# Performance work log

Hardware: AMD Instinct MI355X
Metric: run time of the kernel (lower is better)

Reference implementation:

```python
import jax, jax.numpy as jnp
import numpy as np

E, B, D, T = 8, 4096, 2048, 2048
H = D // 2 + T // 2  # expert hidden dim = 2048
TOP_K = 2


def setup_inputs() -> dict:
    key = jax.random.key(0)
    ks = jax.random.split(key, 5)
    s_in = 1.0 / np.sqrt(D)
    s_h = 1.0 / np.sqrt(H)
    return {
        "xs": jax.random.normal(ks[0], (E, B, D), dtype=jnp.float32),
        "Wg": jax.random.normal(ks[1], (D,), dtype=jnp.float32) * s_in,
        "bg": jnp.zeros((1,), dtype=jnp.float32),
        "W1": jax.random.normal(ks[2], (E, D, H), dtype=jnp.float32) * s_in,
        "b1": jnp.zeros((E, H), dtype=jnp.float32),
        "W2": jax.random.normal(ks[3], (E, H, T), dtype=jnp.float32) * s_h,
        "b2": jnp.zeros((E, T), dtype=jnp.float32),
    }


def reference(xs, Wg, bg, W1, b1, W2, b2):
    # Gating: logits[b, e] = x[e][b] @ Wg + bg  -> [B, E]
    logits = jnp.einsum("ebd,d->be", xs, Wg) + bg
    probs = jax.nn.softmax(logits, axis=1)
    top_k_values, top_k_indices = jax.lax.top_k(probs, TOP_K)  # [B, K]

    # Dense expert compute over each expert's own input stream.
    # hidden[e, b, h] = relu(x[e] @ W1[e] + b1[e]); out[e, b, t] = hidden @ W2[e] + b2[e]
    hidden = jax.nn.relu(jnp.einsum("ebd,edh->ebh", xs, W1) + b1[:, None, :])
    expert_out = jnp.einsum("ebh,eht->ebt", hidden, W2) + b2[:, None, :]  # [E, B, T]

    # Gather the top-k experts per token. In the original, masked-dense compute
    # + output mask is mathematically identical to this gather.
    per_token = jnp.transpose(expert_out, (1, 0, 2))  # [B, E, T]
    selected = jnp.take_along_axis(per_token, top_k_indices[:, :, None], axis=1)  # [B, K, T]

    out = jnp.sum(top_k_values[:, :, None] * selected, axis=1)  # [B, T]
    return out, top_k_values
```

## Files before the change

kernel.cpp:

```cpp
#include <hip/hip_runtime.h>
#include <hip/hip_bf16.h>
#include <stdint.h>

#define E_ 8
#define B_ 4096
#define D_ 2048
#define T_ 2048
#define H_ 2048
#define KDIM 2048
#define NDIM 2048

typedef __attribute__((ext_vector_type(4))) float f32x4;
typedef __attribute__((ext_vector_type(4))) unsigned short u16x4;
typedef __attribute__((ext_vector_type(8))) unsigned short u16x8;
typedef __attribute__((ext_vector_type(8))) __bf16 bf16x8;

__device__ __forceinline__ unsigned short f2bf(float f) {
    __hip_bfloat16 h = __float2bfloat16(f);
    return __builtin_bit_cast(unsigned short, h);
}

__device__ __forceinline__ void gload_lds16(const void* g, void* lds) {
    __builtin_amdgcn_global_load_lds(
        (const __attribute__((address_space(1))) void*)g,
        (__attribute__((address_space(3))) void*)lds, 16, 0, 0);
}

__global__ __launch_bounds__(256) void moe_gating(
    const float* __restrict__ xs, const float* __restrict__ Wg,
    const float* __restrict__ bg, float* __restrict__ out_topk,
    float* __restrict__ prob_slot, int* __restrict__ counts,
    int* __restrict__ slot_of, unsigned short* __restrict__ A1)
{
    const int b = blockIdx.x;
    const int t = threadIdx.x;
    const int wave = t >> 6, lane = t & 63;
    __shared__ float red[E_][4];
    __shared__ int sh_i0, sh_i1;

    const f32x4 wg0 = ((const f32x4*)Wg)[t];
    const f32x4 wg1 = ((const f32x4*)Wg)[t + 256];

    f32x4 xa[E_], xb[E_];
    #pragma unroll
    for (int e = 0; e < E_; ++e) {
        const f32x4* xr = (const f32x4*)(xs + ((size_t)e * B_ + b) * D_);
        xa[e] = __builtin_nontemporal_load(&xr[t]);
        xb[e] = __builtin_nontemporal_load(&xr[t + 256]);
        float p = xa[e].x*wg0.x + xa[e].y*wg0.y + xa[e].z*wg0.z + xa[e].w*wg0.w
                + xb[e].x*wg1.x + xb[e].y*wg1.y + xb[e].z*wg1.z + xb[e].w*wg1.w;
        #pragma unroll
        for (int off = 32; off >= 1; off >>= 1) p += __shfl_xor(p, off);
        if (lane == 0) red[e][wave] = p;
    }
    __syncthreads();
    if (t == 0) {
        float pr[E_];
        float mx = -3.0e38f;
        #pragma unroll
        for (int e = 0; e < E_; ++e) {
            pr[e] = red[e][0] + red[e][1] + red[e][2] + red[e][3] + bg[0];
            mx = fmaxf(mx, pr[e]);
        }
        float s = 0.f;
        #pragma unroll
        for (int e = 0; e < E_; ++e) { pr[e] = expf(pr[e] - mx); s += pr[e]; }
        float inv = 1.0f / s;
        #pragma unroll
        for (int e = 0; e < E_; ++e) pr[e] *= inv;
        int i0 = 0;
        #pragma unroll
        for (int e = 1; e < E_; ++e) if (pr[e] > pr[i0]) i0 = e;
        int i1 = (i0 == 0) ? 1 : 0;
        #pragma unroll
        for (int e = 0; e < E_; ++e) { if (e != i0 && pr[e] > pr[i1]) i1 = e; }
        float p0 = pr[i0], p1 = pr[i1];
        out_topk[2*b]    = p0;
        out_topk[2*b+1]  = p1;
        prob_slot[2*b]   = p0;
        prob_slot[2*b+1] = p1;
        int pos0 = atomicAdd(&counts[i0], 1);
        slot_of[i0 * B_ + pos0] = 2*b;
        int pos1 = atomicAdd(&counts[i1], 1);
        slot_of[i1 * B_ + pos1] = 2*b + 1;
        sh_i0 = i0; sh_i1 = i1;
    }
    __syncthreads();
    const int i0 = sh_i0, i1 = sh_i1;
    f32x4 s0a = xa[0], s0b = xb[0], s1a = xa[0], s1b = xb[0];
    #pragma unroll
    for (int e = 0; e < E_; ++e) {
        if (i0 == e) { s0a = xa[e]; s0b = xb[e]; }
        if (i1 == e) { s1a = xa[e]; s1b = xb[e]; }
    }
    u16x4 w;
    w[0]=f2bf(s0a.x); w[1]=f2bf(s0a.y); w[2]=f2bf(s0a.z); w[3]=f2bf(s0a.w);
    ((u16x4*)(A1 + (size_t)(2*b) * D_))[t] = w;
    w[0]=f2bf(s0b.x); w[1]=f2bf(s0b.y); w[2]=f2bf(s0b.z); w[3]=f2bf(s0b.w);
    ((u16x4*)(A1 + (size_t)(2*b) * D_ + 1024))[t] = w;
    w[0]=f2bf(s1a.x); w[1]=f2bf(s1a.y); w[2]=f2bf(s1a.z); w[3]=f2bf(s1a.w);
    ((u16x4*)(A1 + (size_t)(2*b+1) * D_))[t] = w;
    w[0]=f2bf(s1b.x); w[1]=f2bf(s1b.y); w[2]=f2bf(s1b.z); w[3]=f2bf(s1b.w);
    ((u16x4*)(A1 + (size_t)(2*b+1) * D_ + 1024))[t] = w;
}

__global__ void build_tiles(const int* __restrict__ counts, int* __restrict__ tiles)
{
    if (threadIdx.x == 0 && blockIdx.x == 0) {
        int n = 0;
        for (int e = 0; e < E_; ++e) {
            int te = (counts[e] + 127) >> 7;
            for (int m = 0; m < te; ++m) tiles[1 + n++] = (e << 16) | m;
        }
        tiles[0] = n;
    }
}

template<int DUAL>
__global__ __launch_bounds__(256) void wtrans(
    const float* __restrict__ Wa, const float* __restrict__ Wb,
    unsigned short* __restrict__ Wta, unsigned short* __restrict__ Wtb)
{
    const int z  = blockIdx.z;
    const int e  = DUAL ? (z & 7) : z;
    const float* W = (DUAL && (z >> 3)) ? Wb : Wa;
    unsigned short* Wt = (DUAL && (z >> 3)) ? Wtb : Wta;
    const int kb = blockIdx.x * 64;
    const int nb = blockIdx.y * 64;
    const int t  = threadIdx.x;
    __shared__ float tile[64][68];

    const float* src = W + ((size_t)e * KDIM + kb) * NDIM + nb;
    {
        const int kr = t >> 2, nc = (t & 3) * 16;
        #pragma unroll
        for (int j = 0; j < 4; ++j) {
            f32x4 v = __builtin_nontemporal_load(
                (const f32x4*)(src + (size_t)kr * NDIM + nc + j * 4));
            *(f32x4*)&tile[kr][nc + j * 4] = v;
        }
    }
    __syncthreads();
    {
        const int nn = t >> 2, kc = (t & 3) * 16;
        unsigned short wbuf[16];
        #pragma unroll
        for (int j = 0; j < 16; ++j) wbuf[j] = f2bf(tile[kc + j][nn]);
        unsigned short* dst = Wt + ((size_t)e * NDIM + nb + nn) * KDIM + kb + kc;
        *(u16x8*)dst       = *(const u16x8*)&wbuf[0];
        *((u16x8*)dst + 1) = *(const u16x8*)&wbuf[8];
    }
}

#define BAR  __builtin_amdgcn_s_barrier()

template<int LAYER>
__global__ __launch_bounds__(512, 4) void moe_gemm(
    const unsigned short* __restrict__ Abuf,
    const unsigned short* __restrict__ Wt,
    const float* __restrict__ bias,
    const int* __restrict__ counts,
    const int* __restrict__ tiles,
    const int* __restrict__ slot_of,
    const float* __restrict__ prob_slot,
    unsigned short* __restrict__ hidden_out,
    float* __restrict__ out)
{
    const int nMt = tiles[0];
    const int bid = blockIdx.x;
    const int mt  = bid >> 3;
    const int np  = bid & 7;
    if (mt >= nMt) return;
    const int info = tiles[1 + mt];
    const int e   = info >> 16;
    const int m0  = (info & 0xffff) * 128;
    const int n0  = np * 256;
    const int n_e = counts[e];

    const int t = threadIdx.x;
    const int lane = t & 63;
    const int w = t >> 6;
    const int wm = (w >> 2) * 64;
    const int wn = (w & 3) * 64;
    const int lg = lane >> 4;

    __shared__ u16x8 As[3 * 512];
    __shared__ u16x8 Bs[3 * 1024];
    __shared__ int   slots_s[128];
    __shared__ float probs_s[128];

    if (t < 128) {
        int gm = m0 + t;
        int s = -1; float p = 0.f;
        if (gm < n_e) { s = slot_of[e * B_ + gm]; p = prob_slot[s]; }
        slots_s[t] = s; probs_s[t] = p;
    }
    __syncthreads();

    const int ksw = (((lane & 3) ^ ((lane >> 3) & 3)) << 3);
    const unsigned short* aptr;
    {
        const int r = w * 16 + (lane >> 2);
        int s = slots_s[r]; if (s < 0) s = 0;
        aptr = Abuf + (size_t)s * KDIM + ksw;
    }
    const unsigned short* bptr[2];
    #pragma unroll
    for (int j = 0; j < 2; ++j) {
        const int r = w * 32 + j * 16 + (lane >> 2);
        bptr[j] = Wt + ((size_t)e * NDIM + n0 + r) * KDIM + ksw;
    }

#define STG(BUF, KT) do{ \
    gload_lds16(aptr + (KT)*32,    &As[(BUF)*512  + w*64]); \
    gload_lds16(bptr[0] + (KT)*32, &Bs[(BUF)*1024 + w*128]); \
    gload_lds16(bptr[1] + (KT)*32, &Bs[(BUF)*1024 + w*128 + 64]); }while(0)

    f32x4 acc[4][4];
    #pragma unroll
    for (int i = 0; i < 4; ++i)
        #pragma unroll
        for (int j = 0; j < 4; ++j) {
            f32x4 z = {0.f, 0.f, 0.f, 0.f};
            acc[i][j] = z;
        }

    STG(0, 0); STG(1, 1);

    const int usw = (lane >> 1) & 3;
    int c0 = 0;
    int c2 = 2;
    for (int kt = 0; kt < 64; ++kt) {
        asm volatile("s_waitcnt vmcnt(3)" ::: "memory");
        BAR;
        int tn = kt + 2; if (tn > 63) tn = 63;
        STG(c2, tn);

        const int baseA = c0 * 512;
        const int baseB = c0 * 1024;
        bf16x8 af[4], bq[4];
        #pragma unroll
        for (int mi = 0; mi < 4; ++mi) {
            const int row = wm + mi * 16 + (lane & 15);
            af[mi] = __builtin_bit_cast(bf16x8, As[baseA + row * 4 + (lg ^ usw)]);
        }
        #pragma unroll
        for (int ni = 0; ni < 4; ++ni) {
            const int row = wn + ni * 16 + (lane & 15);
            bq[ni] = __builtin_bit_cast(bf16x8, Bs[baseB + row * 4 + (lg ^ usw)]);
        }
        #pragma unroll
        for (int mi = 0; mi < 4; ++mi)
            #pragma unroll
            for (int ni = 0; ni < 4; ++ni)
                acc[mi][ni] = __builtin_amdgcn_mfma_f32_16x16x32_bf16(
                    af[mi], bq[ni], acc[mi][ni], 0, 0, 0);

        c0 = (c0 == 2) ? 0 : c0 + 1;
        c2 = (c2 == 2) ? 0 : c2 + 1;
    }
    asm volatile("s_waitcnt vmcnt(0)" ::: "memory");

    #pragma unroll
    for (int mi = 0; mi < 4; ++mi) {
        #pragma unroll
        for (int rr = 0; rr < 4; ++rr) {
            const int rloc = wm + mi * 16 + ((lane >> 4) << 2) + rr;
            const int s = slots_s[rloc];
            if (s < 0) continue;
            #pragma unroll
            for (int ni = 0; ni < 4; ++ni) {
                const int col = n0 + wn + ni * 16 + (lane & 15);
                float v = acc[mi][ni][rr];
                if (LAYER == 1) {
                    v += bias[e * NDIM + col];
                    v = fmaxf(v, 0.f);
                    hidden_out[(size_t)s * H_ + col] = f2bf(v);
                } else {
                    v = (v + bias[e * NDIM + col]) * probs_s[rloc];
                    atomicAdd(&out[(size_t)(s >> 1) * T_ + col], v);
                }
            }
        }
    }
#undef STG
}

extern "C" void kernel_launch(void* const* d_in, const int* in_sizes, int n_in,
                              void* d_out, int out_size, void* d_ws, size_t ws_size,
                              hipStream_t stream)
{
    const float* xs = (const float*)d_in[0];
    const float* Wg = (const float*)d_in[1];
    const float* bg = (const float*)d_in[2];
    const float* W1 = (const float*)d_in[3];
    const float* b1 = (const float*)d_in[4];
    const float* W2 = (const float*)d_in[5];
    const float* b2 = (const float*)d_in[6];

    float* out      = (float*)d_out;
    float* out_topk = out + (size_t)B_ * T_;

    char* ws = (char*)d_ws;
    int*   counts    = (int*)ws;
    int*   tiles     = (int*)(ws + 256);
    int*   slot_of   = (int*)(ws + 768);
    float* prob_slot = (float*)(ws + 768 + E_ * B_ * 4);
    size_t off = 768 + (size_t)E_ * B_ * 4 + 2 * B_ * 4;
    off = (off + 255) & ~(size_t)255;
    unsigned short* A1     = (unsigned short*)(ws + off); off += (size_t)2 * B_ * D_ * 2;
    unsigned short* hidden = (unsigned short*)(ws + off); off += (size_t)2 * B_ * H_ * 2;
    unsigned short* Wt1    = (unsigned short*)(ws + off); off += (size_t)E_ * KDIM * NDIM * 2;
    size_t off_big = off + (size_t)E_ * KDIM * NDIM * 2;
    unsigned short* Wt2 = (unsigned short*)(ws + off);

    const bool big = (ws_size >= off_big);

    hipMemsetAsync(counts, 0, 256, stream);
    hipMemsetAsync(out, 0, (size_t)B_ * T_ * sizeof(float), stream);

    dim3 blk(256), gblk(512);
    dim3 ggrid(72 * 8);

    if (big) {
        dim3 tgrid(32, 32, 16);
        wtrans<1><<<tgrid, blk, 0, stream>>>(W1, W2, Wt1, Wt2);
        moe_gating<<<dim3(B_), dim3(256), 0, stream>>>(
            xs, Wg, bg, out_topk, prob_slot, counts, slot_of, A1);
        build_tiles<<<dim3(1), dim3(64), 0, stream>>>(counts, tiles);
        moe_gemm<1><<<ggrid, gblk, 0, stream>>>(
            A1, Wt1, b1, counts, tiles, slot_of, prob_slot, hidden, nullptr);
        moe_gemm<2><<<ggrid, gblk, 0, stream>>>(
            hidden, Wt2, b2, counts, tiles, slot_of, prob_slot, nullptr, out);
    } else {
        dim3 tgrid(32, 32, E_);
        moe_gating<<<dim3(B_), dim3(256), 0, stream>>>(
            xs, Wg, bg, out_topk, prob_slot, counts, slot_of, A1);
        build_tiles<<<dim3(1), dim3(64), 0, stream>>>(counts, tiles);
        wtrans<0><<<tgrid, blk, 0, stream>>>(W1, nullptr, Wt1, nullptr);
        moe_gemm<1><<<ggrid, gblk, 0, stream>>>(
            A1, Wt1, b1, counts, tiles, slot_of, prob_slot, hidden, nullptr);
        wtrans<0><<<tgrid, blk, 0, stream>>>(W2, nullptr, Wt1, nullptr);
        moe_gemm<2><<<ggrid, gblk, 0, stream>>>(
            hidden, Wt1, b2, counts, tiles, slot_of, prob_slot, nullptr, out);
    }
}
```

Before: 542.8 us.

## Pack routed tokens contiguously per expert and retile GEMM with double buffering

Gating no longer writes bf16 activations. A new pack_A kernel gathers each expert's selected token rows into a contiguous per-expert buffer, with token ids and probabilities stored alongside. The GEMM then reads A rows linearly instead of through slot indirection. The GEMM is retiled from 512 threads with a 128x256 tile and a 3-stage 32-wide K pipeline to 256 threads with a 128x128 tile and a 2-stage 64-wide K pipeline using 8-way swizzle. This adds an extra kernel launch and a full re-read of xs, and changes the occupancy and latency-hiding balance.

```diff
diff --git a/kernel.cpp b/kernel.cpp
--- a/kernel.cpp
+++ b/kernel.cpp
@@ -9,6 +9,7 @@
 #define H_ 2048
 #define KDIM 2048
 #define NDIM 2048
+#define NROWS (E_ * 1024 + 128)
 
 typedef __attribute__((ext_vector_type(4))) float f32x4;
 typedef __attribute__((ext_vector_type(4))) unsigned short u16x4;
@@ -30,25 +31,22 @@
     const float* __restrict__ xs, const float* __restrict__ Wg,
     const float* __restrict__ bg, float* __restrict__ out_topk,
     float* __restrict__ prob_slot, int* __restrict__ counts,
-    int* __restrict__ slot_of, unsigned short* __restrict__ A1)
+    int* __restrict__ slot_of)
 {
     const int b = blockIdx.x;
     const int t = threadIdx.x;
     const int wave = t >> 6, lane = t & 63;
     __shared__ float red[E_][4];
-    __shared__ int sh_i0, sh_i1;
 
     const f32x4 wg0 = ((const f32x4*)Wg)[t];
     const f32x4 wg1 = ((const f32x4*)Wg)[t + 256];
 
-    f32x4 xa[E_], xb[E_];
-    #pragma unroll
     for (int e = 0; e < E_; ++e) {
         const f32x4* xr = (const f32x4*)(xs + ((size_t)e * B_ + b) * D_);
-        xa[e] = __builtin_nontemporal_load(&xr[t]);
-        xb[e] = __builtin_nontemporal_load(&xr[t + 256]);
-        float p = xa[e].x*wg0.x + xa[e].y*wg0.y + xa[e].z*wg0.z + xa[e].w*wg0.w
-                + xb[e].x*wg1.x + xb[e].y*wg1.y + xb[e].z*wg1.z + xb[e].w*wg1.w;
+        f32x4 a0 = __builtin_nontemporal_load(&xr[t]);
+        f32x4 a1 = __builtin_nontemporal_load(&xr[t + 256]);
+        float p = a0.x*wg0.x + a0.y*wg0.y + a0.z*wg0.z + a0.w*wg0.w
+                + a1.x*wg1.x + a1.y*wg1.y + a1.z*wg1.z + a1.w*wg1.w;
         #pragma unroll
         for (int off = 32; off >= 1; off >>= 1) p += __shfl_xor(p, off);
         if (lane == 0) red[e][wave] = p;
@@ -83,37 +81,45 @@
         slot_of[i0 * B_ + pos0] = 2*b;
         int pos1 = atomicAdd(&counts[i1], 1);
         slot_of[i1 * B_ + pos1] = 2*b + 1;
-        sh_i0 = i0; sh_i1 = i1;
-    }
-    __syncthreads();
-    const int i0 = sh_i0, i1 = sh_i1;
-    f32x4 s0a = xa[0], s0b = xb[0], s1a = xa[0], s1b = xb[0];
-    #pragma unroll
-    for (int e = 0; e < E_; ++e) {
-        if (i0 == e) { s0a = xa[e]; s0b = xb[e]; }
-        if (i1 == e) { s1a = xa[e]; s1b = xb[e]; }
-    }
-    u16x4 w;
-    w[0]=f2bf(s0a.x); w[1]=f2bf(s0a.y); w[2]=f2bf(s0a.z); w[3]=f2bf(s0a.w);
-    ((u16x4*)(A1 + (size_t)(2*b) * D_))[t] = w;
-    w[0]=f2bf(s0b.x); w[1]=f2bf(s0b.y); w[2]=f2bf(s0b.z); w[3]=f2bf(s0b.w);
-    ((u16x4*)(A1 + (size_t)(2*b) * D_ + 1024))[t] = w;
-    w[0]=f2bf(s1a.x); w[1]=f2bf(s1a.y); w[2]=f2bf(s1a.z); w[3]=f2bf(s1a.w);
-    ((u16x4*)(A1 + (size_t)(2*b+1) * D_))[t] = w;
-    w[0]=f2bf(s1b.x); w[1]=f2bf(s1b.y); w[2]=f2bf(s1b.z); w[3]=f2bf(s1b.w);
-    ((u16x4*)(A1 + (size_t)(2*b+1) * D_ + 1024))[t] = w;
-}
-
-__global__ void build_tiles(const int* __restrict__ counts, int* __restrict__ tiles)
+    }
+}
+
+__global__ void build_tiles(const int* __restrict__ counts,
+                            int* __restrict__ tiles, int* __restrict__ ebase)
 {
     if (threadIdx.x == 0 && blockIdx.x == 0) {
-        int n = 0;
+        int n = 0, base = 0;
         for (int e = 0; e < E_; ++e) {
+            ebase[e] = base;
             int te = (counts[e] + 127) >> 7;
             for (int m = 0; m < te; ++m) tiles[1 + n++] = (e << 16) | m;
+            base += counts[e];
         }
         tiles[0] = n;
     }
+}
+
+__global__ __launch_bounds__(256) void pack_A(
+    const float* __restrict__ xs, const int* __restrict__ slot_of,
+    const int* __restrict__ counts, const int* __restrict__ ebase,
+    const float* __restrict__ prob_slot, unsigned short* __restrict__ Ax,
+    int* __restrict__ tokid, float* __restrict__ prob_pk)
+{
+    const int e = blockIdx.x >> 12;
+    const int i = blockIdx.x & 4095;
+    if (i >= counts[e]) return;
+    const int slot = slot_of[e * B_ + i];
+    const int b = slot >> 1;
+    const int g = ebase[e] + i;
+    const int t = threadIdx.x;
+
+    const f32x4* src = (const f32x4*)(xs + ((size_t)e * B_ + b) * D_);
+    f32x4 v0 = src[2*t], v1 = src[2*t + 1];
+    u16x8 w;
+    w[0]=f2bf(v0.x); w[1]=f2bf(v0.y); w[2]=f2bf(v0.z); w[3]=f2bf(v0.w);
+    w[4]=f2bf(v1.x); w[5]=f2bf(v1.y); w[6]=f2bf(v1.z); w[7]=f2bf(v1.w);
+    ((u16x8*)(Ax + (size_t)g * D_))[t] = w;
+    if (t == 0) { tokid[g] = b; prob_pk[g] = prob_slot[slot]; }
 }
 
 template<int DUAL>
@@ -155,66 +161,51 @@
 #define BAR  __builtin_amdgcn_s_barrier()
 
 template<int LAYER>
-__global__ __launch_bounds__(512, 4) void moe_gemm(
+__global__ __launch_bounds__(256, 2) void moe_gemm(
     const unsigned short* __restrict__ Abuf,
     const unsigned short* __restrict__ Wt,
     const float* __restrict__ bias,
     const int* __restrict__ counts,
     const int* __restrict__ tiles,
-    const int* __restrict__ slot_of,
-    const float* __restrict__ prob_slot,
+    const int* __restrict__ ebase,
+    const int* __restrict__ tokid,
+    const float* __restrict__ prob_pk,
     unsigned short* __restrict__ hidden_out,
     float* __restrict__ out)
 {
     const int nMt = tiles[0];
     const int bid = blockIdx.x;
-    const int mt  = bid >> 3;
-    const int np  = bid & 7;
+    const int mt  = bid >> 4;
+    const int np  = bid & 15;
     if (mt >= nMt) return;
     const int info = tiles[1 + mt];
-    const int e   = info >> 16;
-    const int m0  = (info & 0xffff) * 128;
-    const int n0  = np * 256;
-    const int n_e = counts[e];
+    const int e    = info >> 16;
+    const int mloc = (info & 0xffff) * 128;
+    const int gm0  = ebase[e] + mloc;
+    const int n0   = np * 128;
+    const int n_e  = counts[e];
 
     const int t = threadIdx.x;
     const int lane = t & 63;
     const int w = t >> 6;
-    const int wm = (w >> 2) * 64;
-    const int wn = (w & 3) * 64;
+    const int wm = (w >> 1) * 64;
+    const int wn = (w & 1) * 64;
     const int lg = lane >> 4;
 
-    __shared__ u16x8 As[3 * 512];
-    __shared__ u16x8 Bs[3 * 1024];
-    __shared__ int   slots_s[128];
-    __shared__ float probs_s[128];
-
-    if (t < 128) {
-        int gm = m0 + t;
-        int s = -1; float p = 0.f;
-        if (gm < n_e) { s = slot_of[e * B_ + gm]; p = prob_slot[s]; }
-        slots_s[t] = s; probs_s[t] = p;
-    }
-    __syncthreads();
-
-    const int ksw = (((lane & 3) ^ ((lane >> 3) & 3)) << 3);
-    const unsigned short* aptr;
-    {
-        const int r = w * 16 + (lane >> 2);
-        int s = slots_s[r]; if (s < 0) s = 0;
-        aptr = Abuf + (size_t)s * KDIM + ksw;
-    }
-    const unsigned short* bptr[2];
+    __shared__ u16x8 As[2048];
+    __shared__ u16x8 Bs[2048];
+
+    const int kSrc = (((t & 7) ^ ((t >> 3) & 7)) << 3);
+    const unsigned short* aSrc[4];
+    const unsigned short* bSrc[4];
     #pragma unroll
-    for (int j = 0; j < 2; ++j) {
-        const int r = w * 32 + j * 16 + (lane >> 2);
-        bptr[j] = Wt + ((size_t)e * NDIM + n0 + r) * KDIM + ksw;
-    }
-
-#define STG(BUF, KT) do{ \
-    gload_lds16(aptr + (KT)*32,    &As[(BUF)*512  + w*64]); \
-    gload_lds16(bptr[0] + (KT)*32, &Bs[(BUF)*1024 + w*128]); \
-    gload_lds16(bptr[1] + (KT)*32, &Bs[(BUF)*1024 + w*128 + 64]); }while(0)
+    for (int i = 0; i < 4; ++i) {
+        const int r = i * 32 + (t >> 3);
+        aSrc[i] = Abuf + (size_t)(gm0 + r) * KDIM + kSrc;
+        bSrc[i] = Wt + ((size_t)e * NDIM + n0 + r) * KDIM + kSrc;
+    }
+    u16x8* aDst = &As[0];
+    u16x8* bDst = &Bs[0];
 
     f32x4 acc[4][4];
     #pragma unroll
@@ -225,49 +216,57 @@
             acc[i][j] = z;
         }
 
-    STG(0, 0); STG(1, 1);
-
-    const int usw = (lane >> 1) & 3;
-    int c0 = 0;
-    int c2 = 2;
-    for (int kt = 0; kt < 64; ++kt) {
-        asm volatile("s_waitcnt vmcnt(3)" ::: "memory");
+#define STG(BUF, KT) do{ \
+    _Pragma("unroll") \
+    for (int i = 0; i < 4; ++i) { \
+        gload_lds16(aSrc[i] + (KT)*64, aDst + (BUF)*1024 + t + i*256); \
+        gload_lds16(bSrc[i] + (KT)*64, bDst + (BUF)*1024 + t + i*256); } }while(0)
+
+    STG(0, 0);
+    asm volatile("s_waitcnt vmcnt(0)" ::: "memory");
+    BAR;
+
+    int cur = 0;
+    for (int kt = 0; kt < 32; ++kt) {
+        int tn = kt + 1; if (tn > 31) tn = 31;
+        STG(cur ^ 1, tn);
+
+        #pragma unroll
+        for (int kk = 0; kk < 2; ++kk) {
+            const int kb = kk * 4 + lg;
+            bf16x8 af[4], bq[4];
+            #pragma unroll
+            for (int mi = 0; mi < 4; ++mi) {
+                const int row = wm + mi * 16 + (lane & 15);
+                af[mi] = __builtin_bit_cast(bf16x8,
+                    As[cur * 1024 + row * 8 + (kb ^ (row & 7))]);
+            }
+            #pragma unroll
+            for (int ni = 0; ni < 4; ++ni) {
+                const int row = wn + ni * 16 + (lane & 15);
+                bq[ni] = __builtin_bit_cast(bf16x8,
+                    Bs[cur * 1024 + row * 8 + (kb ^ (row & 7))]);
+            }
+            #pragma unroll
+            for (int mi = 0; mi < 4; ++mi)
+                #pragma unroll
+                for (int ni = 0; ni < 4; ++ni)
+                    acc[mi][ni] = __builtin_amdgcn_mfma_f32_16x16x32_bf16(
+                        af[mi], bq[ni], acc[mi][ni], 0, 0, 0);
+        }
+
+        asm volatile("s_waitcnt vmcnt(0)" ::: "memory");
         BAR;
-        int tn = kt + 2; if (tn > 63) tn = 63;
-        STG(c2, tn);
-
-        const int baseA = c0 * 512;
-        const int baseB = c0 * 1024;
-        bf16x8 af[4], bq[4];
-        #pragma unroll
-        for (int mi = 0; mi < 4; ++mi) {
-            const int row = wm + mi * 16 + (lane & 15);
-            af[mi] = __builtin_bit_cast(bf16x8, As[baseA + row * 4 + (lg ^ usw)]);
-        }
-        #pragma unroll
-        for (int ni = 0; ni < 4; ++ni) {
-            const int row = wn + ni * 16 + (lane & 15);
-            bq[ni] = __builtin_bit_cast(bf16x8, Bs[baseB + row * 4 + (lg ^ usw)]);
-        }
-        #pragma unroll
-        for (int mi = 0; mi < 4; ++mi)
-            #pragma unroll
-            for (int ni = 0; ni < 4; ++ni)
-                acc[mi][ni] = __builtin_amdgcn_mfma_f32_16x16x32_bf16(
-                    af[mi], bq[ni], acc[mi][ni], 0, 0, 0);
-
-        c0 = (c0 == 2) ? 0 : c0 + 1;
-        c2 = (c2 == 2) ? 0 : c2 + 1;
-    }
-    asm volatile("s_waitcnt vmcnt(0)" ::: "memory");
+        cur ^= 1;
+    }
 
     #pragma unroll
     for (int mi = 0; mi < 4; ++mi) {
         #pragma unroll
         for (int rr = 0; rr < 4; ++rr) {
             const int rloc = wm + mi * 16 + ((lane >> 4) << 2) + rr;
-            const int s = slots_s[rloc];
-            if (s < 0) continue;
+            if (mloc + rloc >= n_e) continue;
+            const int g = gm0 + rloc;
             #pragma unroll
             for (int ni = 0; ni < 4; ++ni) {
                 const int col = n0 + wn + ni * 16 + (lane & 15);
@@ -275,10 +274,10 @@
                 if (LAYER == 1) {
                     v += bias[e * NDIM + col];
                     v = fmaxf(v, 0.f);
-                    hidden_out[(size_t)s * H_ + col] = f2bf(v);
+                    hidden_out[(size_t)g * H_ + col] = f2bf(v);
                 } else {
-                    v = (v + bias[e * NDIM + col]) * probs_s[rloc];
-                    atomicAdd(&out[(size_t)(s >> 1) * T_ + col], v);
+                    v = (v + bias[e * NDIM + col]) * prob_pk[g];
+                    atomicAdd(&out[(size_t)tokid[g] * T_ + col], v);
                 }
             }
         }
@@ -304,12 +303,16 @@
     char* ws = (char*)d_ws;
     int*   counts    = (int*)ws;
     int*   tiles     = (int*)(ws + 256);
-    int*   slot_of   = (int*)(ws + 768);
-    float* prob_slot = (float*)(ws + 768 + E_ * B_ * 4);
-    size_t off = 768 + (size_t)E_ * B_ * 4 + 2 * B_ * 4;
+    int*   ebase     = (int*)(ws + 768);
+    int*   slot_of   = (int*)(ws + 1024);
+    float* prob_slot = (float*)(ws + 1024 + E_ * B_ * 4);
+    size_t off = 1024 + (size_t)E_ * B_ * 4 + 2 * B_ * 4;
     off = (off + 255) & ~(size_t)255;
-    unsigned short* A1     = (unsigned short*)(ws + off); off += (size_t)2 * B_ * D_ * 2;
-    unsigned short* hidden = (unsigned short*)(ws + off); off += (size_t)2 * B_ * H_ * 2;
+    int*   tokid   = (int*)(ws + off);   off += (size_t)NROWS * 4;
+    float* prob_pk = (float*)(ws + off); off += (size_t)NROWS * 4;
+    off = (off + 255) & ~(size_t)255;
+    unsigned short* Ax     = (unsigned short*)(ws + off); off += (size_t)NROWS * D_ * 2;
+    unsigned short* hidden = (unsigned short*)(ws + off); off += (size_t)NROWS * H_ * 2;
     unsigned short* Wt1    = (unsigned short*)(ws + off); off += (size_t)E_ * KDIM * NDIM * 2;
     size_t off_big = off + (size_t)E_ * KDIM * NDIM * 2;
     unsigned short* Wt2 = (unsigned short*)(ws + off);
@@ -319,29 +322,34 @@
     hipMemsetAsync(counts, 0, 256, stream);
     hipMemsetAsync(out, 0, (size_t)B_ * T_ * sizeof(float), stream);
 
-    dim3 blk(256), gblk(512);
-    dim3 ggrid(72 * 8);
+    dim3 blk(256);
+    dim3 ggrid(72 * 16);
+    dim3 pgrid(E_ * 4096);
 
     if (big) {
         dim3 tgrid(32, 32, 16);
         wtrans<1><<<tgrid, blk, 0, stream>>>(W1, W2, Wt1, Wt2);
-        moe_gating<<<dim3(B_), dim3(256), 0, stream>>>(
-            xs, Wg, bg, out_topk, prob_slot, counts, slot_of, A1);
-        build_tiles<<<dim3(1), dim3(64), 0, stream>>>(counts, tiles);
-        moe_gemm<1><<<ggrid, gblk, 0, stream>>>(
-            A1, Wt1, b1, counts, tiles, slot_of, prob_slot, hidden, nullptr);
-        moe_gemm<2><<<ggrid, gblk, 0, stream>>>(
-            hidden, Wt2, b2, counts, tiles, slot_of, prob_slot, nullptr, out);
+        moe_gating<<<dim3(B_), blk, 0, stream>>>(
+            xs, Wg, bg, out_topk, prob_slot, counts, slot_of);
+        build_tiles<<<dim3(1), dim3(64), 0, stream>>>(counts, tiles, ebase);
+        pack_A<<<pgrid, blk, 0, stream>>>(
+            xs, slot_of, counts, ebase, prob_slot, Ax, tokid, prob_pk);
+        moe_gemm<1><<<ggrid, blk, 0, stream>>>(
+            Ax, Wt1, b1, counts, tiles, ebase, tokid, prob_pk, hidden, nullptr);
+        moe_gemm<2><<<ggrid, blk, 0, stream>>>(
+            hidden, Wt2, b2, counts, tiles, ebase, tokid, prob_pk, nullptr, out);
     } else {
         dim3 tgrid(32, 32, E_);
-        moe_gating<<<dim3(B_), dim3(256), 0, stream>>>(
-            xs, Wg, bg, out_topk, prob_slot, counts, slot_of, A1);
-        build_tiles<<<dim3(1), dim3(64), 0, stream>>>(counts, tiles);
+        moe_gating<<<dim3(B_), blk, 0, stream>>>(
+            xs, Wg, bg, out_topk, prob_slot, counts, slot_of);
+        build_tiles<<<dim3(1), dim3(64), 0, stream>>>(counts, tiles, ebase);
+        pack_A<<<pgrid, blk, 0, stream>>>(
+            xs, slot_of, counts, ebase, prob_slot, Ax, tokid, prob_pk);
         wtrans<0><<<tgrid, blk, 0, stream>>>(W1, nullptr, Wt1, nullptr);
-        moe_gemm<1><<<ggrid, gblk, 0, stream>>>(
-            A1, Wt1, b1, counts, tiles, slot_of, prob_slot, hidden, nullptr);
+        moe_gemm<1><<<ggrid, blk, 0, stream>>>(
+            Ax, Wt1, b1, counts, tiles, ebase, tokid, prob_pk, hidden, nullptr);
         wtrans<0><<<tgrid, blk, 0, stream>>>(W2, nullptr, Wt1, nullptr);
-        moe_gemm<2><<<ggrid, gblk, 0, stream>>>(
-            hidden, Wt1, b2, counts, tiles, slot_of, prob_slot, nullptr, out);
-    }
-}
+        moe_gemm<2><<<ggrid, blk, 0, stream>>>(
+            hidden, Wt1, b2, counts, tiles, ebase, tokid, prob_pk, nullptr, out);
+    }
+}
```

After: 547.8 us. No clear change (+0.9%).
